# Kernel optimization log

Hardware: AMD Instinct MI355X
Metric: run time of the kernel (lower is better)

## Reference

```python
import jax, jax.numpy as jnp
import numpy as np

EPS = 1e-8


def l2norm(x, axis):
    # matches torch: x / (sqrt(sum(x^2)) + eps)
    return x / (jnp.sqrt(jnp.sum(x * x, axis=axis, keepdims=True)) + EPS)


def setup_inputs() -> dict:
    key = jax.random.key(0)
    k1, k2, k3, k4, k5 = jax.random.split(key, 5)
    I, C, L, R, D = 16, 32, 32, 36, 1024  # n_image, n_caption, max_words, n_regions, embed_dim
    img_emb = l2norm(jax.random.normal(k1, (I, R, D), jnp.float32), -1)
    cap_emb = l2norm(jax.random.normal(k2, (C, L, D), jnp.float32), -1)
    W_emb = jax.random.normal(k3, (D, D), jnp.float32)  # nn.Embedding weight, N(0,1) default init
    sim_map_w = 2.5 + 0.1 * jax.random.normal(k4, (1, D), jnp.float32)  # init_weight: normal(2.5, 0.1)
    temp_scale_w = jnp.full((1, 1), np.log(1.0 / 0.07), jnp.float32)    # init_weight
    temp_learnable_w = jnp.full((1, 1), 4.0, jnp.float32)               # init_weight
    cap_lens = jax.random.randint(k5, (C,), 4, L + 1, jnp.int32)        # ragged caption lengths in [4, L]
    return dict(img_emb=img_emb, cap_emb=cap_emb, W_emb=W_emb, sim_map_w=sim_map_w,
                temp_scale_w=temp_scale_w, temp_learnable_w=temp_learnable_w, cap_lens=cap_lens)


def reference(img_emb, cap_emb, W_emb, sim_map_w, temp_scale_w, temp_learnable_w, cap_lens):
    D = W_emb.shape[0]
    L = cap_emb.shape[1]
    # --- dimension-weight branch (caption-independent) ---
    # linspace(0, D, D).long(): last index is D (out of range in torch); gather with clip.
    idx = jnp.floor(jnp.linspace(0.0, D, D)).astype(jnp.int32)
    weights = jax.nn.sigmoid(jnp.take(W_emb, idx, axis=0, mode='clip'))  # (D, D)
    mean_p = jnp.mean(weights, axis=1)                  # (D,)
    std_p = jnp.std(weights, axis=1, ddof=1)            # torch.std is unbiased
    thres = mean_p + sim_map_w[0] * std_p               # (D,)
    values = jnp.exp(temp_learnable_w[0, 0]) * (weights - thres[:, None])
    mask_p = jnp.tanh(jnp.exp(values))
    Dlw = l2norm(mask_p * weights, axis=1)              # Dim_learned_weights (D, D)
    diag = Dlw.sum(0)                                   # Diagonal (D,); diag_embed matmul == elementwise scale
    smooth = jnp.exp(temp_scale_w[0, 0])
    # --- vectorized ragged per-caption cross attention ---
    wmask = (jnp.arange(L)[None, :] < cap_lens[:, None]).astype(cap_emb.dtype)  # (C, L)
    # attn[c,i,l,r] = tanh(sum_d cap[c,l,d] * diag[d] * img[i,r,d])
    attn = jnp.tanh(jnp.einsum('cld,ird->cilr', cap_emb, img_emb * diag))
    attn = jnp.where(attn >= 0, attn, 0.1 * attn) * wmask[:, None, :, None]  # LeakyReLU(0.1), zero padded words
    attn = attn / (jnp.sqrt(jnp.sum(attn * attn, axis=2, keepdims=True)) + EPS)  # l2norm over word dim
    attn = jax.nn.softmax(attn * smooth, axis=3)        # softmax over regions
    ctx = l2norm(jnp.einsum('cilr,ird->cild', attn, img_emb), axis=-1)  # Context_img
    sim_loc = ctx * cap_emb[:, None, :, :]
    sim_sub = jnp.einsum('cild,ed->cile', sim_loc, Dlw)  # sim_loc @ Dlw.T
    sim_vec = l2norm(sim_sub, axis=-1).sum(-1)           # (C, I, L)
    # mean over the n_word valid words of each caption
    sim = jnp.sum(sim_vec * wmask[:, None, :], axis=2) / cap_lens[:, None].astype(cap_emb.dtype)  # (C, I)
    return sim.T  # (n_image, n_caption), matching torch.cat(sim_all, 1)
```

## Files before the change

kernel.cpp:

```cpp
#include <hip/hip_runtime.h>
#include <hip/hip_bf16.h>

#define I_N 16
#define C_N 32
#define L_N 32
#define R_N 36
#define D_N 1024
#define EPSF 1e-8f

typedef _Float16 f16;
typedef __attribute__((ext_vector_type(8))) _Float16 half8;
typedef __attribute__((ext_vector_type(4))) float floatx4;

__device__ __forceinline__ void gl16(const f16* g, f16* l) {
  __builtin_amdgcn_global_load_lds(
      (const __attribute__((address_space(1))) void*)g,
      (__attribute__((address_space(3))) void*)l, 16, 0, 0);
}

__device__ __forceinline__ float blk_sum_256(float v, float* red) {
  #pragma unroll
  for (int off = 32; off > 0; off >>= 1) v += __shfl_down(v, off, 64);
  int wid = threadIdx.x >> 6;
  if ((threadIdx.x & 63) == 0) red[wid] = v;
  __syncthreads();
  float s = red[0] + red[1] + red[2] + red[3];
  __syncthreads();
  return s;
}

__global__ __launch_bounds__(256) void k_dlw(const float* __restrict__ W,
    const float* __restrict__ simw, const float* __restrict__ tlw,
    float* __restrict__ Dlw, f16* __restrict__ DlwH) {
  int row = blockIdx.x, tid = threadIdx.x;
  __shared__ float red[4];
  const float* Wr = W + (size_t)row * D_N;
  float w[4]; float p = 0.f;
  #pragma unroll
  for (int k = 0; k < 4; ++k) {
    int j = tid + k * 256;
    float x = Wr[j];
    w[k] = 1.f / (1.f + expf(-x));
    p += w[k];
  }
  float S = blk_sum_256(p, red);
  float mean = S * (1.f / 1024.f);
  p = 0.f;
  #pragma unroll
  for (int k = 0; k < 4; ++k) { float d = w[k] - mean; p += d * d; }
  float S2 = blk_sum_256(p, red);
  float stdv = sqrtf(S2 * (1.f / 1023.f));
  float thres = mean + simw[row] * stdv;
  float eT = expf(tlw[0]);
  float mw[4]; p = 0.f;
  #pragma unroll
  for (int k = 0; k < 4; ++k) {
    float val = eT * (w[k] - thres);
    float mp = tanhf(expf(val));
    mw[k] = mp * w[k];
    p += mw[k] * mw[k];
  }
  float S3 = blk_sum_256(p, red);
  float inv = 1.f / (sqrtf(S3) + EPSF);
  #pragma unroll
  for (int k = 0; k < 4; ++k) {
    int j = tid + k * 256;
    float v = mw[k] * inv;
    Dlw[(size_t)row * D_N + j] = v;
    DlwH[(size_t)row * D_N + j] = (f16)v;
  }
}

__global__ __launch_bounds__(256) void k_diag_part(const float* __restrict__ Dlw,
                                                   float* __restrict__ dpart) {
  int col = blockIdx.x * 256 + threadIdx.x;
  int p = blockIdx.y;
  float s = 0.f;
  #pragma unroll 8
  for (int r = p * 64; r < p * 64 + 64; ++r) s += Dlw[(size_t)r * D_N + col];
  dpart[(size_t)p * D_N + col] = s;
}

__global__ __launch_bounds__(256) void k_diag2(const float* __restrict__ dpart,
                                               float* __restrict__ diag) {
  int col = blockIdx.x * 256 + threadIdx.x;
  float s = 0.f;
  #pragma unroll
  for (int p = 0; p < 16; ++p) s += dpart[(size_t)p * D_N + col];
  diag[col] = s;
}

__global__ __launch_bounds__(64) void k_prefix(const int* __restrict__ lens,
                                               int* __restrict__ pfx,
                                               int* __restrict__ mp) {
  int l = threadIdx.x;
  int v = (l < 32) ? lens[l] : 0;
  int s = v;
  #pragma unroll
  for (int off = 1; off < 32; off <<= 1) {
    int t = __shfl_up(s, off, 64);
    if (l >= off) s += t;
  }
  if (l < 32) pfx[l] = s - v;
  if (l == 31) { pfx[32] = s; mp[0] = s * 16; }
}

__global__ __launch_bounds__(256) void k_prep(const float* __restrict__ cap,
    const float* __restrict__ img, const float* __restrict__ diag,
    f16* __restrict__ capH, f16* __restrict__ imgH, f16* __restrict__ imgdH) {
  int bid = blockIdx.x;
  if (bid < 1024) {
    size_t base = (size_t)bid * D_N;
    #pragma unroll
    for (int k = 0; k < 4; ++k) {
      int j = threadIdx.x + k * 256;
      capH[base + j] = (f16)cap[base + j];
    }
  } else if (bid < 1600) {
    size_t base = (size_t)(bid - 1024) * D_N;
    #pragma unroll
    for (int k = 0; k < 4; ++k) {
      int j = threadIdx.x + k * 256;
      imgH[base + j] = (f16)img[base + j];
    }
  } else {
    int row = bid - 1600;
    int i = row / 48, r = row % 48;
    size_t dst = (size_t)row * D_N;
    if (r < R_N) {
      size_t src = ((size_t)i * R_N + r) * D_N;
      #pragma unroll
      for (int k = 0; k < 4; ++k) {
        int j = threadIdx.x + k * 256;
        imgdH[dst + j] = (f16)(img[src + j] * diag[j]);
      }
    } else {
      #pragma unroll
      for (int k = 0; k < 4; ++k) {
        int j = threadIdx.x + k * 256;
        imgdH[dst + j] = (f16)0.f;
      }
    }
  }
}

__global__ __launch_bounds__(256) void k_qk(const f16* __restrict__ A,
    const f16* __restrict__ B, float* __restrict__ qk) {
  int mt = blockIdx.x;
  int i  = blockIdx.y;
  int tid = threadIdx.x;
  int w = tid >> 6, lane = tid & 63;
  int l15 = lane & 15, h = lane >> 4;
  __shared__ __align__(16) f16 Als[64 * 32];
  __shared__ __align__(16) f16 Bls[48 * 32];
  floatx4 acc[3];
  #pragma unroll
  for (int nf = 0; nf < 3; ++nf) acc[nf] = (floatx4)0.f;
  int arow = tid >> 2;
  int u = tid & 3;
  int vf = (u | ((arow & 1) << 2)) ^ ((arow >> 1) & 7);
  int wofs = (((arow & 62) | (vf >> 2)) * 32) + (vf & 3) * 8;
  const f16* Ag = A + (size_t)(mt * 64 + arow) * D_N + u * 8;
  const f16* Bg = B + (size_t)(i * 48 + arow) * D_N + u * 8;
  int v2 = (h | ((l15 & 1) << 2)) ^ ((l15 >> 1) & 7);
  int rbit = (v2 >> 2) & 1;
  int pun = (v2 & 3) * 8;
  int aoff = (w * 16 + (l15 & 14) + rbit) * 32 + pun;
  int boff[3];
  #pragma unroll
  for (int nf = 0; nf < 3; ++nf) boff[nf] = (nf * 16 + (l15 & 14) + rbit) * 32 + pun;
  for (int kk = 0; kk < D_N; kk += 32) {
    *(float4*)(&Als[wofs]) = *(const float4*)(Ag + kk);
    if (tid < 192) *(float4*)(&Bls[wofs]) = *(const float4*)(Bg + kk);
    __syncthreads();
    half8 a = *(const half8*)(&Als[aoff]);
    #pragma unroll
    for (int nf = 0; nf < 3; ++nf) {
      half8 b = *(const half8*)(&Bls[boff[nf]]);
      acc[nf] = __builtin_amdgcn_mfma_f32_16x16x32_f16(a, b, acc[nf], 0, 0, 0);
    }
    __syncthreads();
  }
  #pragma unroll
  for (int nf = 0; nf < 3; ++nf)
    #pragma unroll
    for (int j = 0; j < 4; ++j) {
      int m = mt * 64 + w * 16 + h * 4 + j;
      int n = nf * 16 + l15;
      qk[(size_t)m * 768 + i * 48 + n] = acc[nf][j];
    }
}

__global__ __launch_bounds__(256) void k_attnsm(const float* __restrict__ qk,
    const int* __restrict__ lens, const float* __restrict__ tsw,
    float* __restrict__ pw) {
  int c = blockIdx.x >> 4, i = blockIdx.x & 15;
  int tid = threadIdx.x;
  int len = lens[c];
  float smooth = expf(tsw[0]);
  __shared__ float att[L_N][R_N];
  __shared__ float cn[R_N];
  for (int e = tid; e < L_N * R_N; e += 256) {
    int l = e / R_N, r = e % R_N;
    float x = qk[(size_t)(c * 32 + l) * 768 + i * 48 + r];
    float t = tanhf(x);
    float v = (t >= 0.f) ? t : 0.1f * t;
    if (l >= len) v = 0.f;
    att[l][r] = v;
  }
  __syncthreads();
  if (tid < R_N) {
    float s = 0.f;
    #pragma unroll
    for (int l = 0; l < L_N; ++l) s += att[l][tid] * att[l][tid];
    cn[tid] = sqrtf(s) + EPSF;
  }
  __syncthreads();
  if (tid < L_N) {
    float z[R_N];
    float mx = -3.4e38f;
    #pragma unroll
    for (int r = 0; r < R_N; ++r) { z[r] = att[tid][r] / cn[r] * smooth; mx = fmaxf(mx, z[r]); }
    float se = 0.f;
    #pragma unroll
    for (int r = 0; r < R_N; ++r) { float e = expf(z[r] - mx); z[r] = e; se += e; }
    float inv = 1.f / se;
    #pragma unroll
    for (int r = 0; r < R_N; ++r) att[tid][r] = z[r] * inv;
  }
  __syncthreads();
  for (int e = tid; e < L_N * R_N; e += 256) {
    int l = e / R_N, r = e % R_N;
    pw[((size_t)i * 1024 + c * 32 + l) * R_N + r] = att[l][r];
  }
}

__global__ __launch_bounds__(256) void k_ctx(const float* __restrict__ pw,
    const f16* __restrict__ imgH, const float* __restrict__ cap,
    const int* __restrict__ lens, const int* __restrict__ pfx,
    f16* __restrict__ slc) {
  int mt = blockIdx.x;
  int i  = blockIdx.y;
  int tid = threadIdx.x;
  int w = tid >> 6;
  int cg = tid & 63;
  int c = mt >> 1;
  int lbase = (mt & 1) * 16;
  int len = lens[c];
  int pf = pfx[c];
  __shared__ float pA[16][R_N];
  __shared__ __align__(16) f16 rows[R_N][1024];
  for (int e = tid; e < 16 * R_N; e += 256) {
    int rr = e / R_N, r = e % R_N;
    pA[rr][r] = pw[((size_t)i * 1024 + mt * 16 + rr) * R_N + r];
  }
  const f16* base = imgH + (size_t)i * R_N * D_N;
  #pragma unroll
  for (int t = 0; t < 9; ++t) {
    int rr = w * 9 + t;
    const f16* src = base + (size_t)rr * D_N + cg * 8;
    gl16(src,       &rows[rr][0]);
    gl16(src + 512, &rows[rr][512]);
  }
  __syncthreads();
  float acc[4][16];
  #pragma unroll
  for (int j = 0; j < 4; ++j)
    #pragma unroll
    for (int q = 0; q < 16; ++q) acc[j][q] = 0.f;
  for (int k = 0; k < R_N; ++k) {
    half8 h0 = *(const half8*)(&rows[k][cg * 8]);
    half8 h1 = *(const half8*)(&rows[k][512 + cg * 8]);
    float bv[16];
    #pragma unroll
    for (int q = 0; q < 8; ++q) { bv[q] = (float)h0[q]; bv[8 + q] = (float)h1[q]; }
    #pragma unroll
    for (int j = 0; j < 4; ++j) {
      float a = pA[w * 4 + j][k];
      #pragma unroll
      for (int q = 0; q < 16; ++q) acc[j][q] += a * bv[q];
    }
  }
  int d0 = cg * 8, d1 = 512 + cg * 8;
  #pragma unroll
  for (int j = 0; j < 4; ++j) {
    int l = lbase + w * 4 + j;
    float ss = 0.f;
    #pragma unroll
    for (int q = 0; q < 16; ++q) ss += acc[j][q] * acc[j][q];
    #pragma unroll
    for (int off = 1; off < 64; off <<= 1) ss += __shfl_xor(ss, off, 64);
    if (l < len) {
      float inv = 1.f / (sqrtf(ss) + EPSF);
      const float* capr = cap + ((size_t)c * L_N + l) * D_N;
      float4 c0 = *(const float4*)(capr + d0);
      float4 c1 = *(const float4*)(capr + d0 + 4);
      float4 c2 = *(const float4*)(capr + d1);
      float4 c3 = *(const float4*)(capr + d1 + 4);
      float cv[16] = {c0.x,c0.y,c0.z,c0.w, c1.x,c1.y,c1.z,c1.w,
                      c2.x,c2.y,c2.z,c2.w, c3.x,c3.y,c3.z,c3.w};
      union { f16 h[16]; float4 f4[2]; } u;
      #pragma unroll
      for (int q = 0; q < 16; ++q) u.h[q] = (f16)(acc[j][q] * inv * cv[q]);
      f16* dst = slc + ((size_t)((pf + l) * 16 + i)) * D_N;
      *(float4*)(dst + d0) = u.f4[0];
      *(float4*)(dst + d1) = u.f4[1];
    }
  }
}

__global__ __launch_bounds__(256) void k_gemm(const f16* __restrict__ A,
    const f16* __restrict__ B, const int* __restrict__ mp,
    float* __restrict__ rs16, float* __restrict__ rq16) {
  int bx = blockIdx.x, by = blockIdx.y;
  int Mp = mp[0];
  int m0 = bx * 128, n0 = by * 128;
  if (m0 >= Mp) return;
  int tid = threadIdx.x;
  int w = tid >> 6, lane = tid & 63;
  int l15 = lane & 15, h = lane >> 4;
  int wm = w >> 1, wn = w & 1;
  __shared__ __align__(16) f16 AB[3][2][128 * 32];
  floatx4 acc[4][4];
  #pragma unroll
  for (int mf = 0; mf < 4; ++mf)
    #pragma unroll
    for (int nf = 0; nf < 4; ++nf) acc[mf][nf] = (floatx4)0.f;

  int r_p = lane >> 2, u_p = lane & 3;
  int sw = (r_p >> 1) & 7;
  int val = (u_p | ((r_p & 1) << 2)) ^ sw;
  int r_l = (r_p & 14) | (val >> 2);
  int u_l = val & 3;
  const f16* As0 = A + (size_t)(m0 + w * 32 +  0 + r_l) * D_N + u_l * 8;
  const f16* As1 = A + (size_t)(m0 + w * 32 + 16 + r_l) * D_N + u_l * 8;
  const f16* Bs0 = B + (size_t)(n0 + w * 32 +  0 + r_l) * D_N + u_l * 8;
  const f16* Bs1 = B + (size_t)(n0 + w * 32 + 16 + r_l) * D_N + u_l * 8;

  int v2 = (h | ((l15 & 1) << 2)) ^ ((l15 >> 1) & 7);
  int rbit = (v2 >> 2) & 1;
  int pun = (v2 & 3) * 8;
  int aoff[4], boff[4];
  #pragma unroll
  for (int f = 0; f < 4; ++f) {
    aoff[f] = (wm * 64 + f * 16 + (l15 & 14) + rbit) * 32 + pun;
    boff[f] = (wn * 64 + f * 16 + (l15 & 14) + rbit) * 32 + pun;
  }

  #define STAGE(kt, b) { \
    int kof = (kt) * 32; \
    gl16(As0 + kof, &AB[b][0][(w * 32 +  0) * 32]); \
    gl16(As1 + kof, &AB[b][0][(w * 32 + 16) * 32]); \
    gl16(Bs0 + kof, &AB[b][1][(w * 32 +  0) * 32]); \
    gl16(Bs1 + kof, &AB[b][1][(w * 32 + 16) * 32]); }

  #define COMPUTE(b) { \
    half8 af[4], bf[4]; \
    _Pragma("unroll") for (int f = 0; f < 4; ++f) af[f] = *(const half8*)(&AB[b][0][aoff[f]]); \
    _Pragma("unroll") for (int f = 0; f < 4; ++f) bf[f] = *(const half8*)(&AB[b][1][boff[f]]); \
    _Pragma("unroll") for (int mf = 0; mf < 4; ++mf) \
      _Pragma("unroll") for (int nf = 0; nf < 4; ++nf) \
        acc[mf][nf] = __builtin_amdgcn_mfma_f32_16x16x32_f16(af[mf], bf[nf], acc[mf][nf], 0, 0, 0); }

  STAGE(0, 0);
  STAGE(1, 1);
  int cur = 0, n2 = 2;
  for (int kk = 0; kk < 30; ++kk) {
    STAGE(kk + 2, n2);
    asm volatile("s_waitcnt vmcnt(8)" ::: "memory");
    __builtin_amdgcn_s_barrier();
    __builtin_amdgcn_sched_barrier(0);
    COMPUTE(cur);
    __builtin_amdgcn_s_barrier();
    cur = (cur == 2) ? 0 : cur + 1;
    n2  = (n2  == 2) ? 0 : n2  + 1;
  }
  asm volatile("s_waitcnt vmcnt(4)" ::: "memory");
  __builtin_amdgcn_s_barrier();
  __builtin_amdgcn_sched_barrier(0);
  COMPUTE(cur);
  __builtin_amdgcn_s_barrier();
  cur = (cur == 2) ? 0 : cur + 1;
  asm volatile("s_waitcnt vmcnt(0)" ::: "memory");
  __builtin_amdgcn_s_barrier();
  __builtin_amdgcn_sched_barrier(0);
  COMPUTE(cur);
  #undef STAGE
  #undef COMPUTE

  int slot = by * 2 + wn;
  #pragma unroll
  for (int mf = 0; mf < 4; ++mf)
    #pragma unroll
    for (int j = 0; j < 4; ++j) {
      float s = 0.f, q = 0.f;
      #pragma unroll
      for (int nf = 0; nf < 4; ++nf) { float v = acc[mf][nf][j]; s += v; q += v * v; }
      #pragma unroll
      for (int off = 1; off < 16; off <<= 1) { s += __shfl_xor(s, off, 64); q += __shfl_xor(q, off, 64); }
      if (l15 == 0) {
        int m = m0 + wm * 64 + mf * 16 + h * 4 + j;
        rs16[(size_t)slot * 16384 + m] = s;
        rq16[(size_t)slot * 16384 + m] = q;
      }
    }
}

__global__ __launch_bounds__(64) void k_final(const float* __restrict__ rs16,
    const float* __restrict__ rq16, const int* __restrict__ lens,
    const int* __restrict__ pfx, float* __restrict__ out) {
  int b = blockIdx.x;
  int c = b & 31;
  int l = threadIdx.x;
  int len = lens[c];
  float sv = 0.f;
  if (l < len) {
    int i = b >> 5;
    int row = (pfx[c] + l) * 16 + i;
    float rs = 0.f, rq = 0.f;
    #pragma unroll
    for (int s = 0; s < 16; ++s) {
      rs += rs16[(size_t)s * 16384 + row];
      rq += rq16[(size_t)s * 16384 + row];
    }
    sv = rs / (sqrtf(rq) + EPSF);
  }
  #pragma unroll
  for (int off = 32; off > 0; off >>= 1) sv += __shfl_down(sv, off, 64);
  if (l == 0) out[b] = sv / (float)len;
}

extern "C" void kernel_launch(void* const* d_in, const int* in_sizes, int n_in,
                              void* d_out, int out_size, void* d_ws, size_t ws_size,
                              hipStream_t stream) {
  const float* img  = (const float*)d_in[0];
  const float* cap  = (const float*)d_in[1];
  const float* W    = (const float*)d_in[2];
  const float* simw = (const float*)d_in[3];
  const float* tsw  = (const float*)d_in[4];
  const float* tlw  = (const float*)d_in[5];
  const int*   lens = (const int*)d_in[6];
  float* out = (float*)d_out;

  char* wsB = (char*)d_ws;
  if (ws_size < 51122176) return;
  float* Dlw   = (float*)(wsB + 0);
  f16*   DlwH  = (f16*)  (wsB + 4194304);
  float* diag  = (float*)(wsB + 6291456);
  f16*   capH  = (f16*)  (wsB + 6295552);
  f16*   imgdH = (f16*)  (wsB + 8392704);
  float* qk    = (float*)(wsB + 9965568);
  float* pw    = (float*)(wsB + 13111296);
  f16*   slc   = (f16*)  (wsB + 15470592);
  float* rs16  = (float*)(wsB + 49025024);
  float* rq16  = (float*)(wsB + 50073600);
  float* dpart = qk;
  f16*   imgH  = (f16*)Dlw;
  int*   mp    = (int*)(wsB + 2097152);
  int*   pfx   = (int*)(wsB + 2097152 + 256);

  k_dlw<<<1024, 256, 0, stream>>>(W, simw, tlw, Dlw, DlwH);
  k_diag_part<<<dim3(4, 16), 256, 0, stream>>>(Dlw, dpart);
  k_diag2<<<4, 256, 0, stream>>>(dpart, diag);
  k_prefix<<<1, 64, 0, stream>>>(lens, pfx, mp);
  k_prep<<<2368, 256, 0, stream>>>(cap, img, diag, capH, imgH, imgdH);
  k_qk<<<dim3(16, 16), 256, 0, stream>>>(capH, imgdH, qk);
  k_attnsm<<<512, 256, 0, stream>>>(qk, lens, tsw, pw);
  k_ctx<<<dim3(64, 16), 256, 0, stream>>>(pw, imgH, cap, lens, pfx, slc);
  k_gemm<<<dim3(128, 8), 256, 0, stream>>>(slc, DlwH, mp, rs16, rq16);
  k_final<<<512, 64, 0, stream>>>(rs16, rq16, lens, pfx, out);
}
```

Before: 107.2 us.

## Merge diag/prefix kernels, double ctx rows per block, switch gemm to double-buffer

Fuses the diagonal reduction and caption-length prefix scan into one launch to save a kernel launch. k_ctx now handles all 32 words of a caption per block, so the 72KB image tile staged in LDS is reused twice and half as many blocks are launched. k_gemm drops from triple to double buffering, which lowers LDS use but exposes more load latency per k-step.

Result: slower. 115.0 us (+7.3%).

```diff
diff --git a/kernel.cpp b/kernel.cpp
--- a/kernel.cpp
+++ b/kernel.cpp
@@ -81,28 +81,27 @@
   dpart[(size_t)p * D_N + col] = s;
 }
 
-__global__ __launch_bounds__(256) void k_diag2(const float* __restrict__ dpart,
-                                               float* __restrict__ diag) {
-  int col = blockIdx.x * 256 + threadIdx.x;
-  float s = 0.f;
-  #pragma unroll
-  for (int p = 0; p < 16; ++p) s += dpart[(size_t)p * D_N + col];
-  diag[col] = s;
-}
-
-__global__ __launch_bounds__(64) void k_prefix(const int* __restrict__ lens,
-                                               int* __restrict__ pfx,
-                                               int* __restrict__ mp) {
-  int l = threadIdx.x;
-  int v = (l < 32) ? lens[l] : 0;
-  int s = v;
-  #pragma unroll
-  for (int off = 1; off < 32; off <<= 1) {
-    int t = __shfl_up(s, off, 64);
-    if (l >= off) s += t;
-  }
-  if (l < 32) pfx[l] = s - v;
-  if (l == 31) { pfx[32] = s; mp[0] = s * 16; }
+__global__ __launch_bounds__(256) void k_diag2p(const float* __restrict__ dpart,
+    const int* __restrict__ lens, float* __restrict__ diag,
+    int* __restrict__ pfx, int* __restrict__ mp) {
+  if (blockIdx.x < 4) {
+    int col = blockIdx.x * 256 + threadIdx.x;
+    float s = 0.f;
+    #pragma unroll
+    for (int p = 0; p < 16; ++p) s += dpart[(size_t)p * D_N + col];
+    diag[col] = s;
+  } else if (threadIdx.x < 64) {
+    int l = threadIdx.x;
+    int v = (l < 32) ? lens[l] : 0;
+    int s = v;
+    #pragma unroll
+    for (int off = 1; off < 32; off <<= 1) {
+      int t = __shfl_up(s, off, 64);
+      if (l >= off) s += t;
+    }
+    if (l < 32) pfx[l] = s - v;
+    if (l == 31) { pfx[32] = s; mp[0] = s * 16; }
+  }
 }
 
 __global__ __launch_bounds__(256) void k_prep(const float* __restrict__ cap,
@@ -239,20 +238,18 @@
     const f16* __restrict__ imgH, const float* __restrict__ cap,
     const int* __restrict__ lens, const int* __restrict__ pfx,
     f16* __restrict__ slc) {
-  int mt = blockIdx.x;
+  int c  = blockIdx.x;
   int i  = blockIdx.y;
   int tid = threadIdx.x;
   int w = tid >> 6;
   int cg = tid & 63;
-  int c = mt >> 1;
-  int lbase = (mt & 1) * 16;
   int len = lens[c];
   int pf = pfx[c];
-  __shared__ float pA[16][R_N];
+  __shared__ float pA[32][R_N];
   __shared__ __align__(16) f16 rows[R_N][1024];
-  for (int e = tid; e < 16 * R_N; e += 256) {
+  for (int e = tid; e < 32 * R_N; e += 256) {
     int rr = e / R_N, r = e % R_N;
-    pA[rr][r] = pw[((size_t)i * 1024 + mt * 16 + rr) * R_N + r];
+    pA[rr][r] = pw[((size_t)i * 1024 + c * 32 + rr) * R_N + r];
   }
   const f16* base = imgH + (size_t)i * R_N * D_N;
   #pragma unroll
@@ -263,48 +260,51 @@
     gl16(src + 512, &rows[rr][512]);
   }
   __syncthreads();
-  float acc[4][16];
-  #pragma unroll
-  for (int j = 0; j < 4; ++j)
-    #pragma unroll
-    for (int q = 0; q < 16; ++q) acc[j][q] = 0.f;
-  for (int k = 0; k < R_N; ++k) {
-    half8 h0 = *(const half8*)(&rows[k][cg * 8]);
-    half8 h1 = *(const half8*)(&rows[k][512 + cg * 8]);
-    float bv[16];
-    #pragma unroll
-    for (int q = 0; q < 8; ++q) { bv[q] = (float)h0[q]; bv[8 + q] = (float)h1[q]; }
+  int d0 = cg * 8, d1 = 512 + cg * 8;
+  #pragma unroll
+  for (int sub = 0; sub < 2; ++sub) {
+    float acc[4][16];
+    #pragma unroll
+    for (int j = 0; j < 4; ++j)
+      #pragma unroll
+      for (int q = 0; q < 16; ++q) acc[j][q] = 0.f;
+    for (int k = 0; k < R_N; ++k) {
+      half8 h0 = *(const half8*)(&rows[k][d0]);
+      half8 h1 = *(const half8*)(&rows[k][d1]);
+      float bv[16];
+      #pragma unroll
+      for (int q = 0; q < 8; ++q) { bv[q] = (float)h0[q]; bv[8 + q] = (float)h1[q]; }
+      #pragma unroll
+      for (int j = 0; j < 4; ++j) {
+        float a = pA[sub * 16 + w * 4 + j][k];
+        #pragma unroll
+        for (int q = 0; q < 16; ++q) acc[j][q] += a * bv[q];
+      }
+    }
     #pragma unroll
     for (int j = 0; j < 4; ++j) {
-      float a = pA[w * 4 + j][k];
-      #pragma unroll
-      for (int q = 0; q < 16; ++q) acc[j][q] += a * bv[q];
-    }
-  }
-  int d0 = cg * 8, d1 = 512 + cg * 8;
-  #pragma unroll
-  for (int j = 0; j < 4; ++j) {
-    int l = lbase + w * 4 + j;
-    float ss = 0.f;
-    #pragma unroll
-    for (int q = 0; q < 16; ++q) ss += acc[j][q] * acc[j][q];
-    #pragma unroll
-    for (int off = 1; off < 64; off <<= 1) ss += __shfl_xor(ss, off, 64);
-    if (l < len) {
-      float inv = 1.f / (sqrtf(ss) + EPSF);
-      const float* capr = cap + ((size_t)c * L_N + l) * D_N;
-      float4 c0 = *(const float4*)(capr + d0);
-      float4 c1 = *(const float4*)(capr + d0 + 4);
-      float4 c2 = *(const float4*)(capr + d1);
-      float4 c3 = *(const float4*)(capr + d1 + 4);
-      float cv[16] = {c0.x,c0.y,c0.z,c0.w, c1.x,c1.y,c1.z,c1.w,
-                      c2.x,c2.y,c2.z,c2.w, c3.x,c3.y,c3.z,c3.w};
-      union { f16 h[16]; float4 f4[2]; } u;
-      #pragma unroll
-      for (int q = 0; q < 16; ++q) u.h[q] = (f16)(acc[j][q] * inv * cv[q]);
-      f16* dst = slc + ((size_t)((pf + l) * 16 + i)) * D_N;
-      *(float4*)(dst + d0) = u.f4[0];
-      *(float4*)(dst + d1) = u.f4[1];
+      int l = sub * 16 + w * 4 + j;
+      float ss = 0.f;
+      #pragma unroll
+      for (int q = 0; q < 16; ++q) ss += acc[j][q] * acc[j][q];
+      #pragma unroll
+      for (int off = 1; off < 64; off <<= 1) ss += __shfl_xor(ss, off, 64);
+      if (l < len) {
+        float inv = 1.f / (sqrtf(ss) + EPSF);
+        const float* capr = cap + ((size_t)c * L_N + l) * D_N;
+        float4 c0 = *(const float4*)(capr + d0);
+        float4 c1 = *(const float4*)(capr + d0 + 4);
+        float4 c2 = *(const float4*)(capr + d1);
+        float4 c3 = *(const float4*)(capr + d1 + 4);
+        float cv[16] = {c0.x,c0.y,c0.z,c0.w, c1.x,c1.y,c1.z,c1.w,
+                        c2.x,c2.y,c2.z,c2.w, c3.x,c3.y,c3.z,c3.w};
+        union { f16 h[16]; float4 f4[2]; } u;
+        #pragma unroll
+        for (int q = 0; q < 16; ++q) u.h[q] = (f16)(acc[j][q] * inv * cv[q]);
+        f16* dst = slc + ((size_t)((pf + l) * 16 + i)) * D_N;
+        *(float4*)(dst + d0) = u.f4[0];
+        *(float4*)(dst + d1) = u.f4[1];
+      }
     }
   }
 }
@@ -320,7 +320,7 @@
   int w = tid >> 6, lane = tid & 63;
   int l15 = lane & 15, h = lane >> 4;
   int wm = w >> 1, wn = w & 1;
-  __shared__ __align__(16) f16 AB[3][2][128 * 32];
+  __shared__ __align__(16) f16 AB[2][2][128 * 32];
   floatx4 acc[4][4];
   #pragma unroll
   for (int mf = 0; mf < 4; ++mf)
@@ -363,28 +363,19 @@
         acc[mf][nf] = __builtin_amdgcn_mfma_f32_16x16x32_f16(af[mf], bf[nf], acc[mf][nf], 0, 0, 0); }
 
   STAGE(0, 0);
-  STAGE(1, 1);
-  int cur = 0, n2 = 2;
-  for (int kk = 0; kk < 30; ++kk) {
-    STAGE(kk + 2, n2);
-    asm volatile("s_waitcnt vmcnt(8)" ::: "memory");
+  for (int kk = 0; kk < 31; ++kk) {
+    STAGE(kk + 1, (kk + 1) & 1);
+    asm volatile("s_waitcnt vmcnt(4)" ::: "memory");
     __builtin_amdgcn_s_barrier();
     __builtin_amdgcn_sched_barrier(0);
-    COMPUTE(cur);
+    COMPUTE(kk & 1);
+    __builtin_amdgcn_sched_barrier(0);
     __builtin_amdgcn_s_barrier();
-    cur = (cur == 2) ? 0 : cur + 1;
-    n2  = (n2  == 2) ? 0 : n2  + 1;
-  }
-  asm volatile("s_waitcnt vmcnt(4)" ::: "memory");
-  __builtin_amdgcn_s_barrier();
-  __builtin_amdgcn_sched_barrier(0);
-  COMPUTE(cur);
-  __builtin_amdgcn_s_barrier();
-  cur = (cur == 2) ? 0 : cur + 1;
+  }
   asm volatile("s_waitcnt vmcnt(0)" ::: "memory");
   __builtin_amdgcn_s_barrier();
   __builtin_amdgcn_sched_barrier(0);
-  COMPUTE(cur);
+  COMPUTE(1);
   #undef STAGE
   #undef COMPUTE
 
@@ -461,12 +452,11 @@
 
   k_dlw<<<1024, 256, 0, stream>>>(W, simw, tlw, Dlw, DlwH);
   k_diag_part<<<dim3(4, 16), 256, 0, stream>>>(Dlw, dpart);
-  k_diag2<<<4, 256, 0, stream>>>(dpart, diag);
-  k_prefix<<<1, 64, 0, stream>>>(lens, pfx, mp);
+  k_diag2p<<<5, 256, 0, stream>>>(dpart, lens, diag, pfx, mp);
   k_prep<<<2368, 256, 0, stream>>>(cap, img, diag, capH, imgH, imgdH);
   k_qk<<<dim3(16, 16), 256, 0, stream>>>(capH, imgdH, qk);
   k_attnsm<<<512, 256, 0, stream>>>(qk, lens, tsw, pw);
-  k_ctx<<<dim3(64, 16), 256, 0, stream>>>(pw, imgH, cap, lens, pfx, slc);
+  k_ctx<<<dim3(32, 16), 256, 0, stream>>>(pw, imgH, cap, lens, pfx, slc);
   k_gemm<<<dim3(128, 8), 256, 0, stream>>>(slc, DlwH, mp, rs16, rq16);
   k_final<<<512, 64, 0, stream>>>(rs16, rq16, lens, pfx, out);
 }
```
